# Optimization experiments

Hardware: AMD Instinct MI355X
Metric: run time of the kernel (lower is better)

The kernel has to match this reference:

```python
import math
import jax, jax.numpy as jnp
import numpy as np

H = 1024
N = 64
DT_MIN, DT_MAX = 0.001, 0.1


def setup_inputs() -> dict:
    key = jax.random.key(0)
    k1, k2 = jax.random.split(key)
    # log_dt ~ Uniform[log(dt_min), log(dt_max)]
    log_dt = jax.random.uniform(k1, (H,), dtype=jnp.float32) * (
        math.log(DT_MAX) - math.log(DT_MIN)) + math.log(DT_MIN)
    # C stored as real view of a complex (H, N/2) tensor: last dim = (real, imag)
    C = jax.random.normal(k2, (H, N // 2, 2), dtype=jnp.float32)
    log_A_real = jnp.log(0.5 * jnp.ones((H, N // 2), dtype=jnp.float32))
    A_imag = math.pi * jnp.broadcast_to(
        jnp.arange(N // 2, dtype=jnp.float32)[None, :], (H, N // 2))
    return {"log_dt": log_dt, "C": C, "log_A_real": log_A_real,
            "A_imag": A_imag, "L": 4096}


def reference(log_dt, C, log_A_real, A_imag, L):
    dt = jnp.exp(log_dt)                                   # (H,)
    Cc = jax.lax.complex(C[..., 0], C[..., 1])             # (H, N/2) complex
    A = -jnp.exp(log_A_real) + 1j * A_imag                 # (H, N/2) complex
    dtA = A * dt[:, None]                                  # (H, N/2)
    t = jnp.arange(L, dtype=jnp.float32)                   # (L,)
    K = dtA[:, :, None] * t                                # (H, N/2, L) complex
    Cc = Cc * (jnp.exp(dtA) - 1.0) / A                     # (H, N/2)
    # contract over state dim n; take real part, times 2 (conjugate-pair halves)
    kernel = 2.0 * jnp.einsum('hn,hnl->hl', Cc, jnp.exp(K)).real  # (H, L)
    return kernel
```

## Files before the change

### kernel.cpp

```cpp
#include <hip/hip_runtime.h>


#define NN  32
#define LL  4096
#define TPB 256
#define CH  (LL/TPB)

typedef float f32x2 __attribute__((ext_vector_type(2)));

__global__ __launch_bounds__(TPB, 6) void s4d_kernel(
    const float* __restrict__ log_dt,
    const float* __restrict__ C,
    const float* __restrict__ log_A_real,
    const float* __restrict__ A_imag,
    float* __restrict__ out)
{
    const int h    = blockIdx.x;
    const int lane = threadIdx.x;

    __shared__ float  s_cr[NN], s_ci[NN];
    __shared__ float  s_dtAre[NN];
    __shared__ double s_rev[NN];
    __shared__ float  s_Wr[NN], s_Wi[NN];
    __shared__ float  s_Vr[NN], s_Vi[NN];
    __shared__ float  s_aV[NN], s_mVn[NN];

    if (lane < NN) {
        const int n = lane;
        const float dt    = __expf(log_dt[h]);
        const float Are   = -__expf(log_A_real[h * NN + n]);
        const float Aim   = A_imag[h * NN + n];
        const float dtAre = dt * Are;
        const float dtAim = dt * Aim;

        const float e = __expf(dtAre);
        float s, c;
        __sincosf(dtAim, &s, &c);
        const float nre = e * c - 1.0f;
        const float nim = e * s;
        const float inv = 1.0f / (Are * Are + Aim * Aim);
        const float fre = (nre * Are + nim * Aim) * inv;
        const float fim = (nim * Are - nre * Aim) * inv;

        const float Cre = C[(h * NN + n) * 2 + 0];
        const float Cim = C[(h * NN + n) * 2 + 1];
        s_cr[n] = Cre * fre - Cim * fim;
        s_ci[n] = Cre * fim + Cim * fre;
        s_dtAre[n] = dtAre;

        const double rev1 = (double)dt * (double)Aim * 0.15915494309189535;
        s_rev[n] = rev1;

        double rw = rev1 * (double)TPB;
        rw -= floor(rw);
        float sw, cw;
        __sincosf((float)rw * 6.2831853071795864f, &sw, &cw);
        const float ew = __expf(dtAre * (float)TPB);
        s_Wr[n] = ew * cw;
        s_Wi[n] = ew * sw;

        double rv2 = rev1 * (double)(2 * TPB);
        rv2 -= floor(rv2);
        float sv, cv;
        __sincosf((float)rv2 * 6.2831853071795864f, &sv, &cv);
        const float ew2 = ew * ew;
        s_Vr[n]  = ew2 * cv;
        s_Vi[n]  = ew2 * sv;
        s_aV[n]  = 2.0f * (ew2 * cv);
        s_mVn[n] = -(ew2 * ew2);
    }
    __syncthreads();

    f32x2 acc[CH];
#pragma unroll
    for (int i = 0; i < CH; ++i) acc[i] = (f32x2){0.0f, 0.0f};

    const float lf = (float)lane;

    for (int np = 0; np < NN; np += 2) {
        float E0[2], E1[2], O0[2], O1[2];
#pragma unroll
        for (int jj = 0; jj < 2; ++jj) {
            const int n = np + jj;
            double rv = s_rev[n] * (double)lane;
            rv -= floor(rv);
            float si, co;
            __sincosf((float)rv * 6.2831853071795864f, &si, &co);
            const float er = __expf(s_dtAre[n] * lf);
            const float zr = er * co, zi = er * si;
            const float cr = s_cr[n], cim = s_ci[n];
            const float xr = cr * zr - cim * zi;
            const float xi = cr * zi + cim * zr;
            const float Wr = s_Wr[n], Wi = s_Wi[n];
            const float x1r = xr * Wr - xi * Wi;
            const float x1i = xr * Wi + xi * Wr;
            const float Vr = s_Vr[n], Vi = s_Vi[n];
            E0[jj] = xr;
            E1[jj] = xr * Vr - xi * Vi;
            O0[jj] = x1r;
            O1[jj] = x1r * Vr - x1i * Vi;
        }
        const f32x2 aV  = { s_aV[np],  s_aV[np + 1] };
        const f32x2 mVn = { s_mVn[np], s_mVn[np + 1] };
        f32x2 e0 = { E0[0], E0[1] }, e1 = { E1[0], E1[1] };
        f32x2 o0 = { O0[0], O0[1] }, o1 = { O1[0], O1[1] };
#pragma unroll
        for (int i = 0; i < CH; i += 4) {
            acc[i]     += e0;
            acc[i + 1] += o0;
            acc[i + 2] += e1;
            acc[i + 3] += o1;
            e0 = __builtin_elementwise_fma(aV, e1, mVn * e0);
            o0 = __builtin_elementwise_fma(aV, o1, mVn * o0);
            e1 = __builtin_elementwise_fma(aV, e0, mVn * e1);
            o1 = __builtin_elementwise_fma(aV, o0, mVn * o1);
        }
    }

    float* o = out + (size_t)h * LL + lane;
#pragma unroll
    for (int i = 0; i < CH; ++i)
        o[(size_t)i * TPB] = 2.0f * (acc[i].x + acc[i].y);
}

extern "C" void kernel_launch(void* const* d_in, const int* in_sizes, int n_in,
                              void* d_out, int out_size, void* d_ws, size_t ws_size,
                              hipStream_t stream) {
    const float* log_dt     = (const float*)d_in[0];
    const float* C          = (const float*)d_in[1];
    const float* log_A_real = (const float*)d_in[2];
    const float* A_imag     = (const float*)d_in[3];
    float* out = (float*)d_out;

    const int H = in_sizes[0];
    s4d_kernel<<<dim3(H), dim3(TPB), 0, stream>>>(log_dt, C, log_A_real, A_imag, out);
}
```

Measured before the change: 78.33 us.

## Factor per-lane complex exponentials into two shared-memory lookup tables

The per-thread, per-state double-precision range reduction and sincos/exp, which produced z^lane, is replaced by a product of two 16-entry tables, z^(lane&15) times z^(16*(lane>>4)). The tables are built cooperatively in shared memory after an extra barrier. This takes the transcendental and fp64 work out of the main loop and leaves a complex multiply plus two LDS reads. The launch-bounds occupancy hint also drops from 6 to 4, which loosens register pressure. The trade-offs are more shared memory, another sync, and a small accuracy change from the table product.

```diff
diff --git a/kernel.cpp b/kernel.cpp
--- a/kernel.cpp
+++ b/kernel.cpp
@@ -8,15 +8,15 @@
 
 typedef float f32x2 __attribute__((ext_vector_type(2)));
 
-__global__ __launch_bounds__(TPB, 6) void s4d_kernel(
+__global__ __launch_bounds__(TPB, 4) void s4d_kernel(
     const float* __restrict__ log_dt,
     const float* __restrict__ C,
     const float* __restrict__ log_A_real,
     const float* __restrict__ A_imag,
     float* __restrict__ out)
 {
-    const int h    = blockIdx.x;
-    const int lane = threadIdx.x;
+    const int h = blockIdx.x;
+    const int t = threadIdx.x;
 
     __shared__ float  s_cr[NN], s_ci[NN];
     __shared__ float  s_dtAre[NN];
@@ -24,9 +24,11 @@
     __shared__ float  s_Wr[NN], s_Wi[NN];
     __shared__ float  s_Vr[NN], s_Vi[NN];
     __shared__ float  s_aV[NN], s_mVn[NN];
+    __shared__ f32x2  s_T1[NN][16];
+    __shared__ f32x2  s_T2[NN][16];
 
-    if (lane < NN) {
-        const int n = lane;
+    if (t < NN) {
+        const int n = t;
         const float dt    = __expf(log_dt[h]);
         const float Are   = -__expf(log_A_real[h * NN + n]);
         const float Aim   = A_imag[h * NN + n];
@@ -71,32 +73,54 @@
     }
     __syncthreads();
 
+#pragma unroll
+    for (int rep = 0; rep < 4; ++rep) {
+        const int e = t + rep * TPB;
+        const int n = (e >> 4) & (NN - 1);
+        const int k = e & 15;
+        if (rep < 2) {
+            double rv = s_rev[n] * (double)k;
+            rv -= floor(rv);
+            float si, co;
+            __sincosf((float)rv * 6.2831853071795864f, &si, &co);
+            const float er = __expf(s_dtAre[n] * (float)k);
+            const float zr = er * co, zi = er * si;
+            const float cr = s_cr[n], ci = s_ci[n];
+            s_T1[n][k] = (f32x2){ cr * zr - ci * zi, cr * zi + ci * zr };
+        } else {
+            const int p = k << 4;
+            double rv = s_rev[n] * (double)p;
+            rv -= floor(rv);
+            float si, co;
+            __sincosf((float)rv * 6.2831853071795864f, &si, &co);
+            const float er = __expf(s_dtAre[n] * (float)p);
+            s_T2[n][k] = (f32x2){ er * co, er * si };
+        }
+    }
+    __syncthreads();
+
     f32x2 acc[CH];
 #pragma unroll
     for (int i = 0; i < CH; ++i) acc[i] = (f32x2){0.0f, 0.0f};
 
-    const float lf = (float)lane;
+    const int lo16 = t & 15;
+    const int hi16 = t >> 4;
 
     for (int np = 0; np < NN; np += 2) {
         float E0[2], E1[2], O0[2], O1[2];
 #pragma unroll
         for (int jj = 0; jj < 2; ++jj) {
             const int n = np + jj;
-            double rv = s_rev[n] * (double)lane;
-            rv -= floor(rv);
-            float si, co;
-            __sincosf((float)rv * 6.2831853071795864f, &si, &co);
-            const float er = __expf(s_dtAre[n] * lf);
-            const float zr = er * co, zi = er * si;
-            const float cr = s_cr[n], cim = s_ci[n];
-            const float xr = cr * zr - cim * zi;
-            const float xi = cr * zi + cim * zr;
+            const f32x2 t1 = s_T1[n][lo16];
+            const f32x2 t2 = s_T2[n][hi16];
+            const float zr = t1.x * t2.x - t1.y * t2.y;
+            const float zi = t1.x * t2.y + t1.y * t2.x;
             const float Wr = s_Wr[n], Wi = s_Wi[n];
-            const float x1r = xr * Wr - xi * Wi;
-            const float x1i = xr * Wi + xi * Wr;
+            const float x1r = zr * Wr - zi * Wi;
+            const float x1i = zr * Wi + zi * Wr;
             const float Vr = s_Vr[n], Vi = s_Vi[n];
-            E0[jj] = xr;
-            E1[jj] = xr * Vr - xi * Vi;
+            E0[jj] = zr;
+            E1[jj] = zr * Vr - zi * Vi;
             O0[jj] = x1r;
             O1[jj] = x1r * Vr - x1i * Vi;
         }
@@ -117,7 +141,7 @@
         }
     }
 
-    float* o = out + (size_t)h * LL + lane;
+    float* o = out + (size_t)h * LL + t;
 #pragma unroll
     for (int i = 0; i < CH; ++i)
         o[(size_t)i * TPB] = 2.0f * (acc[i].x + acc[i].y);
```

Measured after the change: 75.55 us. -3.6%, faster.
